# Kernel optimization log

Hardware: AMD Instinct MI355X
Metric: run time of the kernel (lower is better)

## Reference

```python
import jax, jax.numpy as jnp
import numpy as np

MASK_RADIUS = 30.0

def _lowpass_mask(H, W):
    cht, cwt = H // 2, W // 2
    fy = jnp.arange(H, dtype=jnp.float32)[:, None]
    fx = jnp.arange(W, dtype=jnp.float32)[None, :]
    dist = jnp.sqrt((fx - cwt) ** 2 + (fy - cht) ** 2)
    return (dist <= MASK_RADIUS).astype(jnp.float32)

def setup_inputs() -> dict:
    key = jax.random.key(0)
    k1, k2, k3 = jax.random.split(key, 3)
    x = jax.random.normal(k1, (16, 64, 128, 128), dtype=jnp.float32)
    weight = jax.random.normal(k2, (64, 64, 3, 3), dtype=jnp.float32)
    bias = jax.random.normal(k3, (64,), dtype=jnp.float32)
    return {"x": x, "weight": weight, "bias": bias}

def reference(x, weight, bias):
    B, Cin, H, W = x.shape
    # torch.fft.fftshift default shifts ALL dims; jnp default matches.
    fft_x = jnp.fft.fftshift(jnp.fft.fft2(x))                    # [B,Cin,H,W] complex
    kernel_fft = jnp.fft.fftshift(jnp.fft.fft2(weight, s=(H, W)))  # [Cout,Cin,H,W] complex
    # low-pass filter in the shifted frequency domain
    fft_x = fft_x * _lowpass_mask(H, W)
    # channel mixing = batched complex GEMM per frequency (avoids [B,Cout,Cin,H,W] intermediate)
    fft_out = jnp.einsum('bihw,oihw->bohw', fft_x, kernel_fft)
    out = jnp.fft.ifft2(jnp.fft.ifftshift(fft_out, axes=(-2, -1)), axes=(-2, -1)).real
    return out + bias[None, :, None, None]
```

## Files before the change

### kernel.cpp

```cpp
#include <hip/hip_runtime.h>


#define PI2_128 0.04908738521234052f
#define NF 1891

typedef __attribute__((ext_vector_type(8))) short bf16x8;
typedef __attribute__((ext_vector_type(4))) float f32x4;

__device__ const int k_flist[64] = {
    2, 6, 10, 14, 18, 22, 26, 30, 34, 38, 42, 46, 50, 54, 58,
    3, 7, 11, 15, 19, 23, 27, 31, 35, 39, 43, 47, 51, 55, 59,
    0, 4, 8, 12, 16, 20, 24, 28, 32, 36, 40, 44, 48, 52, 56, 60,
    1, 5, 9, 13, 17, 21, 25, 29, 33, 37, 41, 45, 49, 53, 57,
    0, 0, 0};

__device__ inline unsigned bf16_rne(float v) {
  unsigned u = __float_as_uint(v);
  return (u + 0x7FFFu + ((u >> 16) & 1u)) >> 16;
}

__device__ inline bf16x8 mk_bf16x8(unsigned a, unsigned b, unsigned c, unsigned d) {
  union { unsigned u[4]; bf16x8 v; } x;
  x.u[0] = a; x.u[1] = b; x.u[2] = c; x.u[3] = d;
  return x.v;
}

__global__ __launch_bounds__(256) void k012(const float* __restrict__ x,
                                            float* __restrict__ X2,
                                            const float* __restrict__ w,
                                            unsigned* __restrict__ Wt) {
  __shared__ __align__(16) float Cls[8192];
  const int tid = threadIdx.x;

  if (blockIdx.x < 1024) {
    const int bi = blockIdx.x;
    const float* img = x + (size_t)bi * 16384;

    {
      const int tg = tid >> 5;
      const int xg = tid & 31;
      const int t_[4] = {4 * tg, 4 * tg + 2, 2 * tg + 1, 2 * tg + 17};
      const float sgn = (tg & 1) ? 1.f : -1.f;
      float pc[4], ps[4], stc[4], sts[4];
#pragma unroll
      for (int f = 0; f < 4; ++f) {
        __sincosf((float)t_[f] * PI2_128, &sts[f], &stc[f]);
        pc[f] = 1.f;
        ps[f] = 0.f;
      }
      float ar_[4][4] = {{0.f}}, ai_[4][4] = {{0.f}};
      for (int y = 0; y < 32; ++y) {
        float v[4][4];
#pragma unroll
        for (int k = 0; k < 4; ++k)
#pragma unroll
          for (int m = 0; m < 4; ++m) v[k][m] = img[(y + 32 * k) * 128 + xg + 32 * m];
#pragma unroll
        for (int m = 0; m < 4; ++m) {
          float s = v[0][m] + v[2][m], d = v[0][m] - v[2][m];
          float s2 = v[1][m] + v[3][m], d2 = (v[1][m] - v[3][m]) * sgn;
          float a0 = s + s2, a1 = s - s2;
          ar_[0][m] += a0 * pc[0];
          ai_[0][m] -= a0 * ps[0];
          ar_[1][m] += a1 * pc[1];
          ai_[1][m] -= a1 * ps[1];
          ar_[2][m] += d * pc[2] + d2 * ps[2];
          ai_[2][m] += -d * ps[2] + d2 * pc[2];
          ar_[3][m] += d * pc[3] + d2 * ps[3];
          ai_[3][m] += -d * ps[3] + d2 * pc[3];
        }
#pragma unroll
        for (int f = 0; f < 4; ++f) {
          float c = pc[f], s = ps[f];
          pc[f] = c * stc[f] - s * sts[f];
          ps[f] = s * stc[f] + c * sts[f];
        }
      }
      float2* Cf2 = (float2*)Cls;
#pragma unroll
      for (int f = 0; f < 4; ++f) {
        int t = t_[f];
        float Ar = ar_[f][0] + ar_[f][2], Ai = ai_[f][0] + ai_[f][2];
        float Br = ar_[f][0] - ar_[f][2], Bi = ai_[f][0] - ai_[f][2];
        float Cr = ar_[f][1] + ar_[f][3], Ci = ai_[f][1] + ai_[f][3];
        float Dr = ar_[f][1] - ar_[f][3], Di = ai_[f][1] - ai_[f][3];
        const int rowb = xg * 32;
        const int sx = t ^ xg;
        Cf2[0 * 1024 + rowb + (sx ^ 0)] = make_float2(Ar + Cr, Ai + Ci);
        Cf2[1 * 1024 + rowb + (sx ^ 1)] = make_float2(Br + Di, Bi - Dr);
        Cf2[2 * 1024 + rowb + (sx ^ 2)] = make_float2(Ar - Cr, Ai - Ci);
        Cf2[3 * 1024 + rowb + (sx ^ 3)] = make_float2(Br - Di, Bi + Dr);
      }
    }
    __syncthreads();

    {
      const int tg2 = tid >> 5;
      const int fxg = tid & 31;
      float accr[2][4] = {{0.f}}, acci[2][4] = {{0.f}};
      int fxp_[2], r_[2];
      float pc2[2], ps2[2], stc2[2], sts2[2];
#pragma unroll
      for (int u = 0; u < 2; ++u) {
        fxp_[u] = k_flist[2 * fxg + u];
        r_[u] = (fxp_[u] + 2) & 3;
        float fx = (float)(fxp_[u] - 30);
        __sincosf(fx * PI2_128, &sts2[u], &stc2[u]);
        pc2[u] = 1.f;
        ps2[u] = 0.f;
      }
      const float2* Cf2 = (const float2*)Cls;
      const int ts = 4 * tg2;
      for (int xx = 0; xx < 32; ++xx) {
#pragma unroll
        for (int u = 0; u < 2; ++u) {
          const int base = r_[u] * 1024 + xx * 32;
          const int s0 = ts ^ xx ^ r_[u];
          float2 p0 = Cf2[base + s0];
          float2 p1 = Cf2[base + (s0 ^ 1)];
          float2 p2 = Cf2[base + (s0 ^ 2)];
          float2 p3 = Cf2[base + (s0 ^ 3)];
          float zr[4] = {p0.x, p1.x, p2.x, p3.x};
          float zi[4] = {p0.y, p1.y, p2.y, p3.y};
          float c = pc2[u], s = ps2[u];
#pragma unroll
          for (int tt = 0; tt < 4; ++tt) {
            accr[u][tt] += zr[tt] * c + zi[tt] * s;
            acci[u][tt] += zi[tt] * c - zr[tt] * s;
          }
          pc2[u] = c * stc2[u] - s * sts2[u];
          ps2[u] = s * stc2[u] + c * sts2[u];
        }
      }
      float2* X2c = (float2*)X2 + (size_t)bi * NF;
#pragma unroll
      for (int u = 0; u < 2; ++u) {
        if (2 * fxg + u >= 61) continue;
        int fxp = fxp_[u], fx = fxp - 30;
#pragma unroll
        for (int tt = 0; tt < 4; ++tt) {
          int t = 4 * tg2 + tt;
          if (t >= 31) continue;
          bool keep = (t * t + fx * fx) <= 900;
          X2c[fxp * 31 + t] =
              keep ? make_float2(accr[u][tt], acci[u][tt]) : make_float2(0.f, 0.f);
        }
      }
    }
  } else {
    const int bid2 = (int)blockIdx.x - 1024;
    const int fxp = bid2 >> 4;
    const int ig = bid2 & 15;
    const int il = tid & 3;
    const int o = ((tid >> 5) << 3) | ((tid >> 2) & 7);
    const int i = ig * 4 + il;
    const int op = (o + 32) & 63;
    const float* wp = w + (size_t)(op * 64 + i) * 9;
    float w9[9];
#pragma unroll
    for (int k = 0; k < 9; ++k) w9[k] = wp[k];

    const float fx = (float)(fxp - 30);
    float sn, cs;
    __sincosf(fx * PI2_128, &sn, &cs);
    const float e1x = cs, e1y = -sn;
    const float e2x = e1x * e1x - e1y * e1y, e2y = 2.f * e1x * e1y;
    float rxr[3], rxi[3];
#pragma unroll
    for (int ky = 0; ky < 3; ++ky) {
      rxr[ky] = w9[ky * 3] + w9[ky * 3 + 1] * e1x + w9[ky * 3 + 2] * e2x;
      rxi[ky] = w9[ky * 3 + 1] * e1y + w9[ky * 3 + 2] * e2y;
    }
    float pyx = 1.f, pyy = 0.f;
    const float stx = 0.9987954562f, sty = -0.04906767433f;
    unsigned* Wb = Wt + (size_t)(fxp * 31) * 4096 + (o >> 3) * 512 + (i >> 4) * 128 +
                   (((i >> 2) & 3) * 8 + (o & 7)) * 4 + (i & 3);
    for (int fy = 0; fy < 31; ++fy) {
      float p2x = pyx * pyx - pyy * pyy, p2y = 2.f * pyx * pyy;
      float Wre = rxr[0] + (rxr[1] * pyx - rxi[1] * pyy) + (rxr[2] * p2x - rxi[2] * p2y);
      float Wim = rxi[0] + (rxr[1] * pyy + rxi[1] * pyx) + (rxr[2] * p2y + rxi[2] * p2x);
      Wb[(size_t)fy * 4096] = bf16_rne(Wre) | (bf16_rne(Wim) << 16);
      float nx = pyx * stx - pyy * sty;
      pyy = pyx * sty + pyy * stx;
      pyx = nx;
    }
  }
}

__global__ __launch_bounds__(256) void ktx(const float2* __restrict__ X2,
                                           float2* __restrict__ X2T) {
  __shared__ __align__(16) float2 Ld[4096];
  const int tid = threadIdx.x;
  const int tf = blockIdx.x % 30;
  const int tc = blockIdx.x / 30;
  const int f2_0 = tf * 64;
  const int lo = tid & 63, hi = tid >> 6;
#pragma unroll
  for (int k = 0; k < 16; ++k) {
    int c = k * 4 + hi;
    int bi = (c & 15) * 64 + tc * 4 + (c >> 4);
    int f2 = f2_0 + lo;
    float2 v = (f2 < NF) ? X2[(size_t)bi * NF + f2] : make_float2(0.f, 0.f);
    Ld[(c << 6) | (lo ^ c)] = v;
  }
  __syncthreads();
#pragma unroll
  for (int k = 0; k < 16; ++k) {
    int fr = k * 4 + hi;
    int f2 = f2_0 + fr;
    if (f2 < NF) X2T[(size_t)f2 * 1024 + tc * 64 + lo] = Ld[(lo << 6) | (fr ^ lo)];
  }
}

__global__ __launch_bounds__(256) void k3_mfma(const float* X2T,
                                               const unsigned* __restrict__ WtB,
                                               float* F) {
  const int nwg = (int)gridDim.x;
  const int orig = (int)blockIdx.x;
  const int xcd = orig & 7;
  const int q = nwg >> 3, r = nwg & 7;
  const int blk = (xcd < r ? xcd * (q + 1) : r * (q + 1) + (xcd - r) * q) + (orig >> 3);

  const int tid = (int)threadIdx.x;
  const int wv = tid >> 6;
  const int g = blk * 4 + wv;
  const int f2v = g >> 1;
  const bool valid = f2v < NF;
  const int f2 = valid ? f2v : NF - 1;
  const int half = g & 1;
  const int lane = tid & 63;
  const int m = lane & 15;
  const int lg = lane >> 4;
  const int bs = (m + 8) & 15;
  const int co = m & 1;

  float2 xv[4][4];
  const float2* Xc = (const float2*)X2T;
#pragma unroll
  for (int ks = 0; ks < 4; ++ks)
#pragma unroll
    for (int t = 0; t < 4; ++t)
      xv[ks][t] = Xc[(size_t)f2 * 1024 + (ks * 16 + lg * 4 + t) * 16 + bs];

  __syncthreads();

  unsigned ahi[4][4], alo[4][4];
#pragma unroll
  for (int ks = 0; ks < 4; ++ks) {
#pragma unroll
    for (int t = 0; t < 4; ++t) {
      float xr = xv[ks][t].x, xi = xv[ks][t].y;
      unsigned hr = bf16_rne(xr), hi2 = bf16_rne(xi);
      float lr = xr - __uint_as_float(hr << 16);
      float li = xi - __uint_as_float(hi2 << 16);
      ahi[ks][t] = hr | (hi2 << 16);
      alo[ks][t] = bf16_rne(lr) | (bf16_rne(li) << 16);
    }
  }

  f32x4 acc[4];
#pragma unroll
  for (int nt = 0; nt < 4; ++nt) acc[nt] = {0.f, 0.f, 0.f, 0.f};

  const unsigned* Wb =
      WtB + (size_t)f2 * 4096 + half * 2048 + (lg * 8 + (m >> 1)) * 4;
#pragma unroll
  for (int ks = 0; ks < 4; ++ks) {
    bf16x8 bfr[4];
#pragma unroll
    for (int nt = 0; nt < 4; ++nt) {
      uint4 wq = *(const uint4*)(Wb + nt * 512 + ks * 128);
      unsigned b0, b1, b2, b3;
      if (co) {
        b0 = (wq.x >> 16) | (wq.x << 16);
        b1 = (wq.y >> 16) | (wq.y << 16);
        b2 = (wq.z >> 16) | (wq.z << 16);
        b3 = (wq.w >> 16) | (wq.w << 16);
      } else {
        b0 = wq.x ^ 0x80000000u;
        b1 = wq.y ^ 0x80000000u;
        b2 = wq.z ^ 0x80000000u;
        b3 = wq.w ^ 0x80000000u;
      }
      bfr[nt] = mk_bf16x8(b0, b1, b2, b3);
    }
    bf16x8 ah = mk_bf16x8(ahi[ks][0], ahi[ks][1], ahi[ks][2], ahi[ks][3]);
    bf16x8 al = mk_bf16x8(alo[ks][0], alo[ks][1], alo[ks][2], alo[ks][3]);
#pragma unroll
    for (int nt = 0; nt < 4; ++nt)
      acc[nt] = __builtin_amdgcn_mfma_f32_16x16x32_bf16(ah, bfr[nt], acc[nt], 0, 0, 0);
#pragma unroll
    for (int nt = 0; nt < 4; ++nt)
      acc[nt] = __builtin_amdgcn_mfma_f32_16x16x32_bf16(al, bfr[nt], acc[nt], 0, 0, 0);
  }

  if (valid) {
    float* Fo = F + (size_t)f2 * 2048 + half * 64 + m;
#pragma unroll
    for (int nt = 0; nt < 4; ++nt)
#pragma unroll
      for (int rr = 0; rr < 4; ++rr)
        Fo[(lg * 4 + rr) * 128 + nt * 16] = acc[nt][rr];
  }
}

__global__ __launch_bounds__(256) void ktf(const float2* __restrict__ F2,
                                           float2* __restrict__ FT) {
  __shared__ __align__(16) float2 Ld[4096];
  const int tid = threadIdx.x;
  const int tf = blockIdx.x % 30;
  const int tc = blockIdx.x / 30;
  const int f2_0 = tf * 64, c0 = tc * 64;
  const int lo = tid & 63, hi = tid >> 6;
#pragma unroll
  for (int k = 0; k < 16; ++k) {
    int fr = k * 4 + hi;
    int f2 = f2_0 + fr;
    float2 v = (f2 < NF) ? F2[(size_t)f2 * 1024 + c0 + lo] : make_float2(0.f, 0.f);
    Ld[(fr << 6) | (lo ^ fr)] = v;
  }
  __syncthreads();
#pragma unroll
  for (int k = 0; k < 16; ++k) {
    int cc = k * 4 + hi;
    int f2 = f2_0 + lo;
    if (f2 < NF) FT[(size_t)(c0 + cc) * NF + f2] = Ld[(lo << 6) | (cc ^ lo)];
  }
}

__global__ __launch_bounds__(256) void k45_out(const float* __restrict__ FT,
                                               const float* __restrict__ bias,
                                               float* __restrict__ out) {
  __shared__ __align__(16) float2 tw[128];
  __shared__ __align__(16) float U[61 * 132];
  __shared__ __align__(16) float TF[3904];
  const int b = blockIdx.x >> 6;
  const int o = blockIdx.x & 63;
  const int tid = threadIdx.x;
  float2* Fl = (float2*)TF;
  const float2* Fc = (const float2*)FT + (size_t)(b * 64 + o) * NF;
  if (tid < 128) {
    float sv, cv;
    __sincosf((float)tid * PI2_128, &sv, &cv);
    tw[tid] = make_float2(cv, sv);
  }
  for (int j = tid; j < NF; j += 256) Fl[j] = Fc[j];
  __syncthreads();

  {
    const int fy = tid & 31;
    const int xg = tid >> 3 >> 2;
    if (fy < 31) {
      float Sr[4][4] = {{0.f}}, Si[4][4] = {{0.f}};
      float pr[4], pi[4], cr[4], ci[4];
#pragma unroll
      for (int j = 0; j < 4; ++j) {
        int xj = 4 * xg + j;
        float2 st = tw[xj];
        cr[j] = st.x;
        ci[j] = st.y;
        float2 p0 = tw[(-30 * xj) & 127];
        pr[j] = p0.x;
        pi[j] = p0.y;
      }
      const float2* Frow = Fl + fy;
      for (int f4 = 0; f4 < 60; f4 += 4) {
#pragma unroll
        for (int ss = 0; ss < 4; ++ss) {
          const int r = (ss + 2) & 3;
          float2 fv = Frow[(f4 + ss) * 31];
#pragma unroll
          for (int j = 0; j < 4; ++j) {
            Sr[r][j] += fv.x * pr[j] - fv.y * pi[j];
            Si[r][j] += fv.x * pi[j] + fv.y * pr[j];
            float np = pr[j] * cr[j] - pi[j] * ci[j];
            pi[j] = pi[j] * cr[j] + pr[j] * ci[j];
            pr[j] = np;
          }
        }
      }
      {
        float2 fv = Frow[60 * 31];
#pragma unroll
        for (int j = 0; j < 4; ++j) {
          Sr[2][j] += fv.x * pr[j] - fv.y * pi[j];
          Si[2][j] += fv.x * pi[j] + fv.y * pr[j];
        }
      }
#pragma unroll
      for (int j = 0; j < 4; ++j) {
        int xj = 4 * xg + j;
        float Er = Sr[0][j] + Sr[2][j], Ei = Si[0][j] + Si[2][j];
        float Fr = Sr[0][j] - Sr[2][j], Fi = Si[0][j] - Si[2][j];
        float Gr = Sr[1][j] + Sr[3][j], Gi = Si[1][j] + Si[3][j];
        float Hr = Sr[1][j] - Sr[3][j], Hi = Si[1][j] - Si[3][j];
        U[fy * 132 + xj] = Er + Gr;
        U[fy * 132 + xj + 32] = Fr - Hi;
        U[fy * 132 + xj + 64] = Er - Gr;
        U[fy * 132 + xj + 96] = Fr + Hi;
        if (fy >= 1) {
          U[(30 + fy) * 132 + xj] = Ei + Gi;
          U[(30 + fy) * 132 + xj + 32] = Fi + Hr;
          U[(30 + fy) * 132 + xj + 64] = Ei - Gi;
          U[(30 + fy) * 132 + xj + 96] = Fi - Hr;
        }
      }
    }
  }
  __syncthreads();

  {
    const int wv = tid >> 6;
    const int lane = tid & 63;
    const int mm = lane & 15;
    const int kg = lane >> 4;
    const int yA = wv * 16 + mm;
    const float sc1 = 1.f / 16384.f;

    unsigned aPh[4], aPl[4], aQh[4], aQl[4];
#pragma unroll
    for (int pr = 0; pr < 4; ++pr) {
      unsigned hP[2], lP[2], hQ[2], lQ[2];
#pragma unroll
      for (int h2 = 0; h2 < 2; ++h2) {
        int s = pr * 2 + h2;
        int ce = 16 * kg + 2 * s;
        int co = ce + 1;
        float vP, vQ;
        if (ce == 0) vP = sc1;
        else if (ce <= 30) vP = 2.f * sc1 * tw[(ce * yA) & 127].x;
        else if (ce <= 60) vP = -2.f * sc1 * tw[((ce - 30) * yA) & 127].y;
        else vP = 0.f;
        if (co <= 30) vQ = 2.f * sc1 * tw[(co * yA) & 127].x;
        else if (co <= 59) vQ = -2.f * sc1 * tw[((co - 30) * yA) & 127].y;
        else vQ = 0.f;
        unsigned h = bf16_rne(vP);
        hP[h2] = h;
        lP[h2] = bf16_rne(vP - __uint_as_float(h << 16));
        h = bf16_rne(vQ);
        hQ[h2] = h;
        lQ[h2] = bf16_rne(vQ - __uint_as_float(h << 16));
      }
      aPh[pr] = hP[0] | (hP[1] << 16);
      aPl[pr] = lP[0] | (lP[1] << 16);
      aQh[pr] = hQ[0] | (hQ[1] << 16);
      aQl[pr] = lQ[0] | (lQ[1] << 16);
    }
    const bf16x8 APh = mk_bf16x8(aPh[0], aPh[1], aPh[2], aPh[3]);
    const bf16x8 APl = mk_bf16x8(aPl[0], aPl[1], aPl[2], aPl[3]);
    const bf16x8 AQh = mk_bf16x8(aQh[0], aQh[1], aQh[2], aQh[3]);
    const bf16x8 AQl = mk_bf16x8(aQl[0], aQl[1], aQl[2], aQl[3]);

    const float bo_ = bias[o];
    float* op = out + (size_t)(b * 64 + o) * 16384;
#pragma unroll
    for (int n = 0; n < 8; ++n) {
      unsigned uph[4], upl[4], uqh[4], uql[4];
#pragma unroll
      for (int pr = 0; pr < 4; ++pr) {
        unsigned h0[2], l0[2], h1[2], l1[2];
#pragma unroll
        for (int h2 = 0; h2 < 2; ++h2) {
          int s = pr * 2 + h2;
          int ce = 16 * kg + 2 * s;
          int rP = ce > 60 ? 60 : ce;
          int rQ = (ce + 1) > 60 ? 60 : ce + 1;
          float uP = U[rP * 132 + n * 16 + mm];
          float uQ = U[rQ * 132 + n * 16 + mm];
          unsigned h = bf16_rne(uP);
          h0[h2] = h;
          l0[h2] = bf16_rne(uP - __uint_as_float(h << 16));
          h = bf16_rne(uQ);
          h1[h2] = h;
          l1[h2] = bf16_rne(uQ - __uint_as_float(h << 16));
        }
        uph[pr] = h0[0] | (h0[1] << 16);
        upl[pr] = l0[0] | (l0[1] << 16);
        uqh[pr] = h1[0] | (h1[1] << 16);
        uql[pr] = l1[0] | (l1[1] << 16);
      }
      bf16x8 UPh = mk_bf16x8(uph[0], uph[1], uph[2], uph[3]);
      bf16x8 UPl = mk_bf16x8(upl[0], upl[1], upl[2], upl[3]);
      bf16x8 UQh = mk_bf16x8(uqh[0], uqh[1], uqh[2], uqh[3]);
      bf16x8 UQl = mk_bf16x8(uql[0], uql[1], uql[2], uql[3]);
      f32x4 accP = {0.f, 0.f, 0.f, 0.f}, accQ = {0.f, 0.f, 0.f, 0.f};
      accP = __builtin_amdgcn_mfma_f32_16x16x32_bf16(APh, UPh, accP, 0, 0, 0);
      accP = __builtin_amdgcn_mfma_f32_16x16x32_bf16(APh, UPl, accP, 0, 0, 0);
      accP = __builtin_amdgcn_mfma_f32_16x16x32_bf16(APl, UPh, accP, 0, 0, 0);
      accQ = __builtin_amdgcn_mfma_f32_16x16x32_bf16(AQh, UQh, accQ, 0, 0, 0);
      accQ = __builtin_amdgcn_mfma_f32_16x16x32_bf16(AQh, UQl, accQ, 0, 0, 0);
      accQ = __builtin_amdgcn_mfma_f32_16x16x32_bf16(AQl, UQh, accQ, 0, 0, 0);
#pragma unroll
      for (int rr = 0; rr < 4; ++rr) {
        int y = wv * 16 + kg * 4 + rr;
        float p = accP[rr], qq = accQ[rr];
        op[y * 128 + n * 16 + mm] = p + qq + bo_;
        op[(y + 64) * 128 + n * 16 + mm] = p - qq + bo_;
      }
    }
  }
}

extern "C" void kernel_launch(void* const* d_in, const int* in_sizes, int n_in,
                              void* d_out, int out_size, void* d_ws, size_t ws_size,
                              hipStream_t stream) {
  (void)in_sizes; (void)n_in; (void)out_size; (void)ws_size;
  const float* x = (const float*)d_in[0];
  const float* w = (const float*)d_in[1];
  const float* bias = (const float*)d_in[2];
  float* out = (float*)d_out;

  unsigned* Wt = (unsigned*)d_ws;
  float* A = (float*)d_ws + 7745536;
  float* B = (float*)d_ws + 11618304;

  k012<<<2000, 256, 0, stream>>>(x, A, w, Wt);
  ktx<<<480, 256, 0, stream>>>((const float2*)A, (float2*)B);
  k3_mfma<<<946, 256, 0, stream>>>(B, Wt, B);
  ktf<<<480, 256, 0, stream>>>((const float2*)B, (float2*)A);
  k45_out<<<1024, 256, 0, stream>>>(A, bias, out);
}
```

Baseline: 219.8 us.

## Compute second DFT stage with split-bf16 MFMA instead of scalar FMA loop

Measured after the change: 214.9 us. -2.2%, faster.

```diff
diff --git a/kernel.cpp b/kernel.cpp
--- a/kernel.cpp
+++ b/kernel.cpp
@@ -95,57 +95,95 @@
     __syncthreads();
 
     {
-      const int tg2 = tid >> 5;
-      const int fxg = tid & 31;
-      float accr[2][4] = {{0.f}}, acci[2][4] = {{0.f}};
-      int fxp_[2], r_[2];
-      float pc2[2], ps2[2], stc2[2], sts2[2];
-#pragma unroll
-      for (int u = 0; u < 2; ++u) {
-        fxp_[u] = k_flist[2 * fxg + u];
-        r_[u] = (fxp_[u] + 2) & 3;
-        float fx = (float)(fxp_[u] - 30);
-        __sincosf(fx * PI2_128, &sts2[u], &stc2[u]);
-        pc2[u] = 1.f;
-        ps2[u] = 0.f;
-      }
+      const int wv = tid >> 6;
+      const int lane = tid & 63;
+      const int mm = lane & 15;
+      const int kg = lane >> 4;
+      const int secS[4] = {0, 15, 30, 46};
+      const int secC[4] = {15, 15, 16, 15};
+      const int r = wv;
+      const int cnt = secC[r];
+      const int mc = mm < cnt ? mm : cnt - 1;
+      const int fxpA = k_flist[secS[r] + mc];
+      const float fx = (float)(fxpA - 30);
+
+      unsigned ARh[2][4], ARl[2][4], AIh[2][4], AIl[2][4];
+#pragma unroll
+      for (int ks = 0; ks < 2; ++ks)
+#pragma unroll
+        for (int q = 0; q < 4; ++q) {
+          int xx = ks * 16 + kg * 4 + q;
+          float sv, cv;
+          __sincosf(fx * (float)xx * PI2_128, &sv, &cv);
+          unsigned ch = bf16_rne(cv), sh = bf16_rne(sv);
+          float cl = cv - __uint_as_float(ch << 16);
+          float sl = sv - __uint_as_float(sh << 16);
+          unsigned chl = bf16_rne(cl), shl = bf16_rne(sl);
+          ARh[ks][q] = ch | (sh << 16);
+          ARl[ks][q] = chl | (shl << 16);
+          AIh[ks][q] = (sh ^ 0x8000u) | (ch << 16);
+          AIl[ks][q] = (shl ^ 0x8000u) | (chl << 16);
+        }
+
       const float2* Cf2 = (const float2*)Cls;
-      const int ts = 4 * tg2;
-      for (int xx = 0; xx < 32; ++xx) {
-#pragma unroll
-        for (int u = 0; u < 2; ++u) {
-          const int base = r_[u] * 1024 + xx * 32;
-          const int s0 = ts ^ xx ^ r_[u];
-          float2 p0 = Cf2[base + s0];
-          float2 p1 = Cf2[base + (s0 ^ 1)];
-          float2 p2 = Cf2[base + (s0 ^ 2)];
-          float2 p3 = Cf2[base + (s0 ^ 3)];
-          float zr[4] = {p0.x, p1.x, p2.x, p3.x};
-          float zi[4] = {p0.y, p1.y, p2.y, p3.y};
-          float c = pc2[u], s = ps2[u];
-#pragma unroll
-          for (int tt = 0; tt < 4; ++tt) {
-            accr[u][tt] += zr[tt] * c + zi[tt] * s;
-            acci[u][tt] += zi[tt] * c - zr[tt] * s;
+      f32x4 accR0 = {0.f, 0.f, 0.f, 0.f}, accR1 = {0.f, 0.f, 0.f, 0.f};
+      f32x4 accI0 = {0.f, 0.f, 0.f, 0.f}, accI1 = {0.f, 0.f, 0.f, 0.f};
+#pragma unroll
+      for (int ks = 0; ks < 2; ++ks) {
+        bf16x8 Arh = mk_bf16x8(ARh[ks][0], ARh[ks][1], ARh[ks][2], ARh[ks][3]);
+        bf16x8 Arl = mk_bf16x8(ARl[ks][0], ARl[ks][1], ARl[ks][2], ARl[ks][3]);
+        bf16x8 Aih = mk_bf16x8(AIh[ks][0], AIh[ks][1], AIh[ks][2], AIh[ks][3]);
+        bf16x8 Ail = mk_bf16x8(AIl[ks][0], AIl[ks][1], AIl[ks][2], AIl[ks][3]);
+#pragma unroll
+        for (int nt = 0; nt < 2; ++nt) {
+          unsigned bh[4], bl[4];
+#pragma unroll
+          for (int q = 0; q < 4; ++q) {
+            int xx = ks * 16 + kg * 4 + q;
+            int t = nt * 16 + mm;
+            float2 z = Cf2[r * 1024 + xx * 32 + (t ^ xx ^ r)];
+            unsigned zrh = bf16_rne(z.x), zih = bf16_rne(z.y);
+            float zrl = z.x - __uint_as_float(zrh << 16);
+            float zil = z.y - __uint_as_float(zih << 16);
+            bh[q] = zrh | (zih << 16);
+            bl[q] = bf16_rne(zrl) | (bf16_rne(zil) << 16);
           }
-          pc2[u] = c * stc2[u] - s * sts2[u];
-          ps2[u] = s * stc2[u] + c * sts2[u];
-        }
-      }
+          bf16x8 Bh = mk_bf16x8(bh[0], bh[1], bh[2], bh[3]);
+          bf16x8 Bl = mk_bf16x8(bl[0], bl[1], bl[2], bl[3]);
+          if (nt == 0) {
+            accR0 = __builtin_amdgcn_mfma_f32_16x16x32_bf16(Arh, Bh, accR0, 0, 0, 0);
+            accR0 = __builtin_amdgcn_mfma_f32_16x16x32_bf16(Arh, Bl, accR0, 0, 0, 0);
+            accR0 = __builtin_amdgcn_mfma_f32_16x16x32_bf16(Arl, Bh, accR0, 0, 0, 0);
+            accI0 = __builtin_amdgcn_mfma_f32_16x16x32_bf16(Aih, Bh, accI0, 0, 0, 0);
+            accI0 = __builtin_amdgcn_mfma_f32_16x16x32_bf16(Aih, Bl, accI0, 0, 0, 0);
+            accI0 = __builtin_amdgcn_mfma_f32_16x16x32_bf16(Ail, Bh, accI0, 0, 0, 0);
+          } else {
+            accR1 = __builtin_amdgcn_mfma_f32_16x16x32_bf16(Arh, Bh, accR1, 0, 0, 0);
+            accR1 = __builtin_amdgcn_mfma_f32_16x16x32_bf16(Arh, Bl, accR1, 0, 0, 0);
+            accR1 = __builtin_amdgcn_mfma_f32_16x16x32_bf16(Arl, Bh, accR1, 0, 0, 0);
+            accI1 = __builtin_amdgcn_mfma_f32_16x16x32_bf16(Aih, Bh, accI1, 0, 0, 0);
+            accI1 = __builtin_amdgcn_mfma_f32_16x16x32_bf16(Aih, Bl, accI1, 0, 0, 0);
+            accI1 = __builtin_amdgcn_mfma_f32_16x16x32_bf16(Ail, Bh, accI1, 0, 0, 0);
+          }
+        }
+      }
+
       float2* X2c = (float2*)X2 + (size_t)bi * NF;
 #pragma unroll
-      for (int u = 0; u < 2; ++u) {
-        if (2 * fxg + u >= 61) continue;
-        int fxp = fxp_[u], fx = fxp - 30;
-#pragma unroll
-        for (int tt = 0; tt < 4; ++tt) {
-          int t = 4 * tg2 + tt;
-          if (t >= 31) continue;
-          bool keep = (t * t + fx * fx) <= 900;
-          X2c[fxp * 31 + t] =
-              keep ? make_float2(accr[u][tt], acci[u][tt]) : make_float2(0.f, 0.f);
-        }
-      }
+      for (int nt = 0; nt < 2; ++nt)
+#pragma unroll
+        for (int rr = 0; rr < 4; ++rr) {
+          int mp = kg * 4 + rr;
+          int t = nt * 16 + mm;
+          if (mp < cnt && t <= 30) {
+            int fxpw = k_flist[secS[r] + mp];
+            int fxv = fxpw - 30;
+            bool keep = (t * t + fxv * fxv) <= 900;
+            float re = nt == 0 ? accR0[rr] : accR1[rr];
+            float im = nt == 0 ? accI0[rr] : accI1[rr];
+            X2c[fxpw * 31 + t] = keep ? make_float2(re, im) : make_float2(0.f, 0.f);
+          }
+        }
     }
   } else {
     const int bid2 = (int)blockIdx.x - 1024;
```
